# Kernel optimization log

Hardware: AMD Instinct MI355X
Metric: run time of the kernel (lower is better)

## Reference

```python
import jax, jax.numpy as jnp
import numpy as np

N = 100000
E = 1600000
IN, HID, OUT = 128, 256, 128


def setup_inputs() -> dict:
    key = jax.random.key(0)
    ks = jax.random.split(key, 8)
    x = jax.random.normal(ks[0], (N, IN), dtype=jnp.float32)
    edge_index = jax.random.randint(ks[1], (2, E), 0, N, dtype=jnp.int64)
    # PyG SAGEConv params: lin_l (neighbor aggr, with bias), lin_r (root, no bias)
    def glorot(k, shape):
        fan_in = shape[1]
        return jax.random.normal(k, shape, dtype=jnp.float32) / jnp.sqrt(jnp.float32(fan_in))
    W1l = glorot(ks[2], (HID, IN)); b1 = jnp.zeros((HID,), jnp.float32)
    W1r = glorot(ks[3], (HID, IN))
    W2l = glorot(ks[4], (OUT, HID)); b2 = jnp.zeros((OUT,), jnp.float32)
    W2r = glorot(ks[5], (OUT, HID))
    return {"x": x, "edge_index": edge_index, "W1l": W1l, "b1": b1,
            "W1r": W1r, "W2l": W2l, "b2": b2, "W2r": W2r}


def sage_conv(x, row, col, Wl, b, Wr, n_nodes):
    # mean-aggregate neighbor features x[row] at target nodes col
    msg = x[row]                                               # [E, d]
    s = jax.ops.segment_sum(msg, col, num_segments=n_nodes)    # [N, d]
    deg = jax.ops.segment_sum(jnp.ones((row.shape[0], 1), x.dtype), col,
                              num_segments=n_nodes)            # [N, 1]
    mean = s / jnp.maximum(deg, 1.0)
    return mean @ Wl.T + b + x @ Wr.T


def reference(x, edge_index, W1l, b1, W1r, W2l, b2, W2r):
    row, col = edge_index[0], edge_index[1]
    h = sage_conv(x, row, col, W1l, b1, W1r, N)
    h = jax.nn.relu(h)
    # dropout is identity in eval mode
    out = sage_conv(h, row, col, W2l, b2, W2r, N)
    return out
```

## Files before the change

### kernel.cpp

```cpp
#include <hip/hip_runtime.h>
#include <hip/hip_bf16.h>
#include <hip/hip_fp16.h>

#define NN 100000
#define NE 1600000
#define NCHUNK ((NN + 127) / 128)
#define NPB 512
#define NB 256
#define CHUNK 8192
#define NCH ((NE + CHUNK - 1) / CHUNK)

typedef __attribute__((ext_vector_type(8))) short short8;
typedef __attribute__((ext_vector_type(4))) float float4v;
typedef __attribute__((ext_vector_type(2))) float float2v;

__device__ __forceinline__ unsigned short f2bf(float f) {
    unsigned int b = __float_as_uint(f);
    return (unsigned short)((b + 0x7fffu + ((b >> 16) & 1u)) >> 16);
}
__device__ __forceinline__ unsigned int pack_bf16(float lo, float hi) {
    return (unsigned int)f2bf(lo) | ((unsigned int)f2bf(hi) << 16);
}
__device__ __forceinline__ unsigned char f2fp8(float v) {
    int r = __builtin_amdgcn_cvt_pk_fp8_f32(v, v, 0, false);
    return (unsigned char)(r & 0xff);
}
__device__ __forceinline__ unsigned short pack2fp8(float lo, float hi) {
    int r = __builtin_amdgcn_cvt_pk_fp8_f32(lo, hi, 0, false);
    return (unsigned short)(r & 0xffff);
}
__device__ __forceinline__ float h2f(unsigned short u) {
    return __half2float(__ushort_as_half(u));
}

__global__ void k_prep(const float* x, const float* W1l, const float* W1r,
                       const float* W2l, const float* W2r, const int* ei,
                       unsigned int* axb_u, unsigned short* xf8, unsigned short* wb1,
                       unsigned short* wb2, int* bcnt, unsigned short* gz) {
    __shared__ int hh[NB];
    int b = blockIdx.x, t = threadIdx.x;
    if (b < 3125) {
#pragma unroll
        for (int k = 0; k < 8; k++) {
            int tt = b * 2048 + k * 256 + t;
            int node = tt >> 6, i = tt & 63;
            float2 v = ((const float2*)x)[tt];
            axb_u[(size_t)node * 128 + 64 + i] = pack_bf16(v.x, v.y);
            xf8[(size_t)node * 64 + i] = pack2fp8(v.x, v.y);
        }
    } else if (b < 3253) {
        int i = (b - 3125) * 256 + t;
        int r1 = i >> 7, c1 = i & 127;
        wb1[r1 * 256 + c1]       = f2bf(W1l[i]);
        wb1[r1 * 256 + 128 + c1] = f2bf(W1r[i]);
        wb2[i]         = f2bf(W2l[i]);
        wb2[32768 + i] = f2bf(W2r[i]);
    } else if (b < 3509) {
        hh[t] = 0;
        __syncthreads();
        int e0 = (b - 3253) * 6250;
        for (int e = e0 + t; e < e0 + 6250; e += 256)
            atomicAdd(&hh[ei[NE + e] >> 9], 1);
        __syncthreads();
        if (hh[t]) atomicAdd(&bcnt[t], hh[t]);
    } else {
        if (t < 64) xf8[(size_t)NN * 64 + t] = 0;
        else if (t < 128 && gz) gz[(size_t)NN * 64 + (t - 64)] = 0;
    }
}

__global__ void k_bscan(const int* bcnt, int* boff, int* bcur) {
    __shared__ int s[NB];
    int t = threadIdx.x;
    int v = bcnt[t];
    s[t] = v;
    __syncthreads();
    for (int d = 1; d < NB; d <<= 1) {
        int val = (t >= d) ? s[t - d] : 0;
        __syncthreads();
        s[t] += val;
        __syncthreads();
    }
    boff[t + 1] = s[t];
    if (t == 0) boff[0] = 0;
    bcur[t] = s[t] - v;
}

__global__ __launch_bounds__(256) void k_bscatter(const int* ei, int* bcur, unsigned int* pairs) {
    __shared__ unsigned int buf[CHUNK];
    __shared__ int cnt[NB];
    __shared__ int lbase[NB];
    __shared__ int lcur[NB];
    __shared__ int gpos[NB];
    int t = threadIdx.x;
    int e0 = blockIdx.x * CHUNK;
    int nedge = NE - e0; if (nedge > CHUNK) nedge = CHUNK;
    cnt[t] = 0;
    __syncthreads();
    for (int i = t; i < nedge; i += 256)
        atomicAdd(&cnt[ei[NE + e0 + i] >> 9], 1);
    __syncthreads();
    int v = cnt[t];
    lcur[t] = v;
    __syncthreads();
    for (int d = 1; d < NB; d <<= 1) {
        int val = (t >= d) ? lcur[t - d] : 0;
        __syncthreads();
        lcur[t] += val;
        __syncthreads();
    }
    lbase[t] = lcur[t] - v;
    gpos[t] = atomicAdd(&bcur[t], v);
    __syncthreads();
    lcur[t] = lbase[t];
    __syncthreads();
    for (int i = t; i < nedge; i += 256) {
        int r = ei[e0 + i], c = ei[NE + e0 + i];
        int b = c >> 9;
        int p = atomicAdd(&lcur[b], 1);
        buf[p] = (unsigned)r | ((unsigned)(c & 511) << 17);
    }
    __syncthreads();
    int wv = t >> 6, lane = t & 63;
    for (int b = wv; b < NB; b += 4) {
        int n = cnt[b], lb = lbase[b], gp = gpos[b];
        for (int i = lane; i < n; i += 64)
            pairs[gp + i] = buf[lb + i];
    }
}

__global__ __launch_bounds__(256) void k_build(const unsigned int* pairs, const int* boff,
                                               int* off, int* deg, int* csr, int* csr32) {
    __shared__ int ldeg[NPB];
    __shared__ int lcur[NPB];
    __shared__ int lini[NPB];
    __shared__ int sscan[256];
    int b = blockIdx.x;
    int nbase = b * NPB;
    if (nbase >= NN) return;
    int t = threadIdx.x;
    int base = boff[b], cntb = boff[b + 1] - base;
    ldeg[t] = 0; ldeg[t + 256] = 0;
    __syncthreads();
    for (int i = t; i < cntb; i += 256) {
        unsigned int pr = pairs[base + i];
        atomicAdd(&ldeg[pr >> 17], 1);
    }
    __syncthreads();
    int d0 = ldeg[2 * t], d1 = ldeg[2 * t + 1];
    int v = d0 + d1;
    sscan[t] = v;
    __syncthreads();
    for (int d = 1; d < 256; d <<= 1) {
        int val = (t >= d) ? sscan[t - d] : 0;
        __syncthreads();
        sscan[t] += val;
        __syncthreads();
    }
    int ex = sscan[t] - v;
    lcur[2 * t] = ex;      lcur[2 * t + 1] = ex + d0;
    lini[2 * t] = ex;      lini[2 * t + 1] = ex + d0;
    __syncthreads();
    int nloc = NN - nbase; if (nloc > NPB) nloc = NPB;
    for (int ln = t; ln < nloc; ln += 256) {
        off[nbase + ln] = base + lcur[ln];
        deg[nbase + ln] = ldeg[ln];
    }
    __syncthreads();
    if (csr32) {
        for (int i = t; i < cntb; i += 256) {
            unsigned int pr = pairs[base + i];
            int nd = pr >> 17;
            int p = atomicAdd(&lcur[nd], 1);
            int src = (int)(pr & 0x1FFFFu);
            csr[base + p] = src;
            int rk = p - lini[nd];
            if (rk < 32) csr32[(size_t)(nbase + nd) * 32 + rk] = src;
        }
    } else {
        for (int i = t; i < cntb; i += 256) {
            unsigned int pr = pairs[base + i];
            int p = atomicAdd(&lcur[pr >> 17], 1);
            csr[base + p] = (int)(pr & 0x1FFFFu);
        }
    }
}

__global__ __launch_bounds__(512) void k_agg1(const unsigned short* xf8, const int* off,
                                              const int* deg, const int* csr, const int* csr32,
                                              unsigned int* axb_w) {
    int wid = (blockIdx.x * 512 + threadIdx.x) >> 6;
    if (wid >= NN) return;
    int widu = __builtin_amdgcn_readfirstlane(wid);
    int lane = threadIdx.x & 63;
    int d = deg[widu];
    float a0 = 0.f, a1 = 0.f;
    if (csr32) {
        const int* c32 = csr32 + (size_t)widu * 32;
        int dm = d < 32 ? d : 32;
#pragma unroll
        for (int r = 0; r < 32; r++) {
            int idx = (r < dm) ? c32[r] : NN;
            unsigned short u = xf8[(size_t)idx * 64 + lane];
            float2v f = __builtin_amdgcn_cvt_pk_f32_fp8((unsigned int)u, false);
            a0 += f.x; a1 += f.y;
        }
        if (d > 32) {
            int start = off[widu];
            for (int j = 32; j < d; j++) {
                int idx = csr[start + j];
                unsigned short u = xf8[(size_t)idx * 64 + lane];
                float2v f = __builtin_amdgcn_cvt_pk_f32_fp8((unsigned int)u, false);
                a0 += f.x; a1 += f.y;
            }
        }
    } else {
        int start = off[widu];
        for (int j = 0; j < d; j++) {
            int idx = csr[start + j];
            unsigned short u = xf8[(size_t)idx * 64 + lane];
            float2v f = __builtin_amdgcn_cvt_pk_f32_fp8((unsigned int)u, false);
            a0 += f.x; a1 += f.y;
        }
    }
    float inv = 1.0f / (float)(d > 0 ? d : 1);
    axb_w[(size_t)wid * 128 + lane] = pack_bf16(a0 * inv, a1 * inv);
}

__global__ __launch_bounds__(512) void k_agg2(const unsigned short* g, const int* off,
                                              const int* deg, const int* csr, const int* csr32,
                                              const unsigned short* partial, float* out) {
    int wid = (blockIdx.x * 512 + threadIdx.x) >> 6;
    if (wid >= NN) return;
    int widu = __builtin_amdgcn_readfirstlane(wid);
    int lane = threadIdx.x & 63;
    int d = deg[widu];
    unsigned int pu = *(const unsigned int*)(partial + (size_t)widu * 128 + (lane << 1));
    float a0 = 0.f, a1 = 0.f;
    if (csr32) {
        const int* c32 = csr32 + (size_t)widu * 32;
        int dm = d < 32 ? d : 32;
#pragma unroll
        for (int r = 0; r < 32; r++) {
            int idx = (r < dm) ? c32[r] : NN;
            unsigned short u = g[(size_t)idx * 64 + lane];
            float2v f = __builtin_amdgcn_cvt_pk_f32_fp8((unsigned int)u, false);
            a0 += f.x; a1 += f.y;
        }
        if (d > 32) {
            int start = off[widu];
            for (int j = 32; j < d; j++) {
                int idx = csr[start + j];
                unsigned short u = g[(size_t)idx * 64 + lane];
                float2v f = __builtin_amdgcn_cvt_pk_f32_fp8((unsigned int)u, false);
                a0 += f.x; a1 += f.y;
            }
        }
    } else {
        int start = off[widu];
        for (int j = 0; j < d; j++) {
            int idx = csr[start + j];
            unsigned short u = g[(size_t)idx * 64 + lane];
            float2v f = __builtin_amdgcn_cvt_pk_f32_fp8((unsigned int)u, false);
            a0 += f.x; a1 += f.y;
        }
    }
    float inv = 1.0f / (float)(d > 0 ? d : 1);
    float2 o;
    o.x = h2f((unsigned short)(pu & 0xffff)) + a0 * inv;
    o.y = h2f((unsigned short)(pu >> 16)) + a1 * inv;
    *(float2*)(out + (size_t)wid * 128 + (lane << 1)) = o;
}

#define BROW 264
#define GGRID (32 * ((NCHUNK + 7) / 8))
__global__ __launch_bounds__(256, 4) void k_gemm1(const unsigned short* A, const unsigned short* wb,
                                                  const float* b1, unsigned short* H) {
    __shared__ unsigned short Bs[64 * BROW];
    int t = threadIdx.x;
    int b = blockIdx.x;
    int chunk = (b & 7) + ((b >> 5) << 3);
    int cg = (b >> 3) & 3;
    if (chunk >= NCHUNK) return;
    {
        const short8* src = (const short8*)(wb + (size_t)cg * 64 * 256);
        short8* dst = (short8*)Bs;
#pragma unroll
        for (int i = 0; i < 8; i++) {
            int gi = i * 256 + t;
            int r = gi >> 5, c = gi & 31;
            dst[r * 33 + c] = src[gi];
        }
    }
    __syncthreads();
    int wv = t >> 6, lane = t & 63;
    int mrow = lane & 15, quad = lane >> 4;
    int base = chunk * 128 + wv * 32;
    if (base >= NN) return;
    float bias[4];
#pragma unroll
    for (int ctl = 0; ctl < 4; ctl++) bias[ctl] = b1[cg * 64 + ctl * 16 + mrow];
    float4v acc[2][4];
#pragma unroll
    for (int h = 0; h < 2; h++)
#pragma unroll
        for (int ctl = 0; ctl < 4; ctl++) acc[h][ctl] = (float4v)(0.0f);
    const short8* a0p = (const short8*)(A + (size_t)(base + mrow) * 256);
    const short8* a1p = (const short8*)(A + (size_t)(base + 16 + mrow) * 256);
#pragma unroll
    for (int kk = 0; kk < 8; kk++) {
        short8 a0 = a0p[kk * 4 + quad];
        short8 a1 = a1p[kk * 4 + quad];
        int koff = kk * 32 + quad * 8;
#pragma unroll
        for (int ctl = 0; ctl < 4; ctl++) {
            short8 bfr = *(const short8*)(Bs + (ctl * 16 + mrow) * BROW + koff);
            acc[0][ctl] = __builtin_amdgcn_mfma_f32_16x16x32_bf16(a0, bfr, acc[0][ctl], 0, 0, 0);
            acc[1][ctl] = __builtin_amdgcn_mfma_f32_16x16x32_bf16(a1, bfr, acc[1][ctl], 0, 0, 0);
        }
    }
#pragma unroll
    for (int ctl = 0; ctl < 4; ctl++) {
        int col = cg * 64 + ctl * 16 + mrow;
#pragma unroll
        for (int h = 0; h < 2; h++)
#pragma unroll
            for (int r = 0; r < 4; r++) {
                int node = base + h * 16 + quad * 4 + r;
                float v = acc[h][ctl][r] + bias[ctl];
                H[(size_t)node * 256 + col] = f2bf(fmaxf(v, 0.f));
            }
    }
}

__global__ __launch_bounds__(256, 4) void k_gemm2(const unsigned short* A, const unsigned short* wb,
                                                  const float* b2, unsigned char* g,
                                                  unsigned short* partial) {
    __shared__ unsigned short Bs[64 * BROW];
    int t = threadIdx.x;
    int b = blockIdx.x;
    int chunk = (b & 7) + ((b >> 5) << 3);
    int cg = (b >> 3) & 3;
    if (chunk >= NCHUNK) return;
    {
        const short8* src = (const short8*)(wb + (size_t)cg * 64 * 256);
        short8* dst = (short8*)Bs;
#pragma unroll
        for (int i = 0; i < 8; i++) {
            int gi = i * 256 + t;
            int r = gi >> 5, c = gi & 31;
            dst[r * 33 + c] = src[gi];
        }
    }
    __syncthreads();
    int wv = t >> 6, lane = t & 63;
    int mrow = lane & 15, quad = lane >> 4;
    int base = chunk * 128 + wv * 32;
    if (base >= NN) return;
    float bias[4];
#pragma unroll
    for (int ctl = 0; ctl < 4; ctl++)
        bias[ctl] = (cg >= 2) ? b2[cg * 64 + ctl * 16 + mrow - 128] : 0.f;
    float4v acc[2][4];
#pragma unroll
    for (int h = 0; h < 2; h++)
#pragma unroll
        for (int ctl = 0; ctl < 4; ctl++) acc[h][ctl] = (float4v)(0.0f);
    const short8* a0p = (const short8*)(A + (size_t)(base + mrow) * 256);
    const short8* a1p = (const short8*)(A + (size_t)(base + 16 + mrow) * 256);
#pragma unroll
    for (int kk = 0; kk < 8; kk++) {
        short8 a0 = a0p[kk * 4 + quad];
        short8 a1 = a1p[kk * 4 + quad];
        int koff = kk * 32 + quad * 8;
#pragma unroll
        for (int ctl = 0; ctl < 4; ctl++) {
            short8 bfr = *(const short8*)(Bs + (ctl * 16 + mrow) * BROW + koff);
            acc[0][ctl] = __builtin_amdgcn_mfma_f32_16x16x32_bf16(a0, bfr, acc[0][ctl], 0, 0, 0);
            acc[1][ctl] = __builtin_amdgcn_mfma_f32_16x16x32_bf16(a1, bfr, acc[1][ctl], 0, 0, 0);
        }
    }
    if (cg < 2) {
#pragma unroll
        for (int ctl = 0; ctl < 4; ctl++) {
            int col = cg * 64 + ctl * 16 + mrow;
#pragma unroll
            for (int h = 0; h < 2; h++)
#pragma unroll
                for (int r = 0; r < 4; r++) {
                    int node = base + h * 16 + quad * 4 + r;
                    g[(size_t)node * 128 + col] = f2fp8(acc[h][ctl][r]);
                }
        }
    } else {
#pragma unroll
        for (int ctl = 0; ctl < 4; ctl++) {
            int pcol = cg * 64 + ctl * 16 + mrow - 128;
#pragma unroll
            for (int h = 0; h < 2; h++)
#pragma unroll
                for (int r = 0; r < 4; r++) {
                    int node = base + h * 16 + quad * 4 + r;
                    __half hf = __float2half(acc[h][ctl][r] + bias[ctl]);
                    partial[(size_t)node * 128 + pcol] = __half_as_ushort(hf);
                }
        }
    }
}

extern "C" void kernel_launch(void* const* d_in, const int* in_sizes, int n_in,
                              void* d_out, int out_size, void* d_ws, size_t ws_size,
                              hipStream_t stream) {
    const float* x   = (const float*)d_in[0];
    const int*   ei  = (const int*)d_in[1];
    const float* W1l = (const float*)d_in[2];
    const float* b1  = (const float*)d_in[3];
    const float* W1r = (const float*)d_in[4];
    const float* W2l = (const float*)d_in[5];
    const float* b2  = (const float*)d_in[6];
    const float* W2r = (const float*)d_in[7];
    float* out = (float*)d_out;

    char* p = (char*)d_ws;
    unsigned int* axb = (unsigned int*)p; p += (size_t)NN * 256 * 2;
    unsigned short* h = (unsigned short*)p; p += (size_t)NN * 256 * 2;
    unsigned char* g  = (unsigned char*)p; p += (size_t)NN * 128 + 256;
    unsigned short* xf8 = (unsigned short*)p; p += (size_t)NN * 128 + 256;
    unsigned short* wb1 = (unsigned short*)p; p += 65536 * 2;
    unsigned short* wb2 = (unsigned short*)p; p += 65536 * 2;
    int* deg  = (int*)p; p += (size_t)NN * 4;
    int* off  = (int*)p; p += (size_t)NN * 4;
    int* csr  = (int*)p; p += (size_t)NE * 4;
    int* bcnt = (int*)p; p += NB * 4;
    int* boff = (int*)p; p += (NB + 1) * 4;
    int* bcur = (int*)p; p += NB * 4;
    if (ws_size < (size_t)(p - (char*)d_ws)) return;
    int* csr32 = (int*)p; p += (size_t)NN * 32 * 4;
    if (ws_size < (size_t)(p - (char*)d_ws)) csr32 = nullptr;
    unsigned int* pairs = (unsigned int*)h;
    unsigned short* partial = (unsigned short*)axb;

    hipMemsetAsync(bcnt, 0, NB * 4, stream);
    k_prep<<<3510, 256, 0, stream>>>(x, W1l, W1r, W2l, W2r, ei, axb, xf8, wb1, wb2, bcnt,
                                     (unsigned short*)g);
    k_bscan<<<1, NB, 0, stream>>>(bcnt, boff, bcur);
    k_bscatter<<<NCH, 256, 0, stream>>>(ei, bcur, pairs);
    k_build<<<NB, 256, 0, stream>>>(pairs, boff, off, deg, csr, csr32);
    k_agg1<<<12500, 512, 0, stream>>>(xf8, off, deg, csr, csr32, axb);
    k_gemm1<<<GGRID, 256, 0, stream>>>((const unsigned short*)axb, wb1, b1, h);
    k_gemm2<<<GGRID, 256, 0, stream>>>(h, wb2, b2, g, partial);
    k_agg2<<<12500, 512, 0, stream>>>((const unsigned short*)g, off, deg, csr, csr32, partial, out);
}
```

Before: 362.3 us.

## Slice fp8 feature tables into column slabs for cache-local neighbor gathers

Stores the fp8 node features (input x and layer-2 g) as four 32-byte column slices, each a separate contiguous array. Aggregation kernels now use 16 lanes per node and 4 nodes per wave, with block IDs interleaved so neighbouring blocks gather from the same slice, shrinking the working set per slice so it fits in cache. Neighbour indices are loaded once per lane and broadcast with shuffles, and streaming loads and stores are marked nontemporal. The partial-sum layout is also sliced to match. The csr32-absent fallback is removed, so correctness now assumes the workspace is large enough for csr32.

```diff
diff --git a/kernel.cpp b/kernel.cpp
--- a/kernel.cpp
+++ b/kernel.cpp
@@ -4,6 +4,7 @@
 
 #define NN 100000
 #define NE 1600000
+#define NNP (NN + 8)
 #define NCHUNK ((NN + 127) / 128)
 #define NPB 512
 #define NB 256
@@ -14,6 +15,9 @@
 typedef __attribute__((ext_vector_type(4))) float float4v;
 typedef __attribute__((ext_vector_type(2))) float float2v;
 
+#define SLS ((size_t)NNP * 16)
+#define NN32 ((size_t)NN * 32)
+
 __device__ __forceinline__ unsigned short f2bf(float f) {
     unsigned int b = __float_as_uint(f);
     return (unsigned short)((b + 0x7fffu + ((b >> 16) & 1u)) >> 16);
@@ -35,8 +39,8 @@
 
 __global__ void k_prep(const float* x, const float* W1l, const float* W1r,
                        const float* W2l, const float* W2r, const int* ei,
-                       unsigned int* axb_u, unsigned short* xf8, unsigned short* wb1,
-                       unsigned short* wb2, int* bcnt, unsigned short* gz) {
+                       unsigned int* axb_u, unsigned short* xf8s, unsigned short* wb1,
+                       unsigned short* wb2, int* bcnt, unsigned short* g2z) {
     __shared__ int hh[NB];
     int b = blockIdx.x, t = threadIdx.x;
     if (b < 3125) {
@@ -46,7 +50,7 @@
             int node = tt >> 6, i = tt & 63;
             float2 v = ((const float2*)x)[tt];
             axb_u[(size_t)node * 128 + 64 + i] = pack_bf16(v.x, v.y);
-            xf8[(size_t)node * 64 + i] = pack2fp8(v.x, v.y);
+            xf8s[(size_t)(i >> 4) * SLS + (size_t)node * 16 + (i & 15)] = pack2fp8(v.x, v.y);
         }
     } else if (b < 3253) {
         int i = (b - 3125) * 256 + t;
@@ -64,8 +68,11 @@
         __syncthreads();
         if (hh[t]) atomicAdd(&bcnt[t], hh[t]);
     } else {
-        if (t < 64) xf8[(size_t)NN * 64 + t] = 0;
-        else if (t < 128 && gz) gz[(size_t)NN * 64 + (t - 64)] = 0;
+        if (t < 64) xf8s[(size_t)(t >> 4) * SLS + (size_t)NN * 16 + (t & 15)] = 0;
+        else if (t < 128) {
+            int q = t - 64;
+            g2z[(size_t)(q >> 4) * SLS + (size_t)NN * 16 + (q & 15)] = 0;
+        }
     }
 }
 
@@ -186,90 +193,88 @@
     }
 }
 
-__global__ __launch_bounds__(512) void k_agg1(const unsigned short* xf8, const int* off,
+__global__ __launch_bounds__(512) void k_agg1(const unsigned short* xs, const int* off,
                                               const int* deg, const int* csr, const int* csr32,
                                               unsigned int* axb_w) {
-    int wid = (blockIdx.x * 512 + threadIdx.x) >> 6;
-    if (wid >= NN) return;
-    int widu = __builtin_amdgcn_readfirstlane(wid);
-    int lane = threadIdx.x & 63;
-    int d = deg[widu];
+    int bid = blockIdx.x;
+    int s = (bid & 7) >> 1;
+    int k = ((bid >> 3) << 1) | (bid & 1);
+    if (k >= 3125) return;
+    int t = threadIdx.x;
+    int lane = t & 63;
+    int grp = lane >> 4, l16 = lane & 15;
+    int node = k * 32 + (t >> 6) * 4 + grp;
+    const unsigned short* gs = xs + (size_t)s * SLS;
+    int d = deg[node];
+    const int* c32 = csr32 + (size_t)node * 32;
+    int e0 = __builtin_nontemporal_load(c32 + l16);
+    int e1 = __builtin_nontemporal_load(c32 + 16 + l16);
+    int dm = d < 32 ? d : 32;
     float a0 = 0.f, a1 = 0.f;
-    if (csr32) {
-        const int* c32 = csr32 + (size_t)widu * 32;
-        int dm = d < 32 ? d : 32;
-#pragma unroll
-        for (int r = 0; r < 32; r++) {
-            int idx = (r < dm) ? c32[r] : NN;
-            unsigned short u = xf8[(size_t)idx * 64 + lane];
+#pragma unroll
+    for (int slot = 0; slot < 32; slot++) {
+        int idx = __shfl(slot < 16 ? e0 : e1, (grp << 4) | (slot & 15), 64);
+        idx = (slot < dm) ? idx : NN;
+        unsigned short u = gs[(size_t)idx * 16 + l16];
+        float2v f = __builtin_amdgcn_cvt_pk_f32_fp8((unsigned int)u, false);
+        a0 += f.x; a1 += f.y;
+    }
+    if (d > 32) {
+        int st = off[node];
+        for (int j = 32; j < d; j++) {
+            int idx = csr[st + j];
+            unsigned short u = gs[(size_t)idx * 16 + l16];
             float2v f = __builtin_amdgcn_cvt_pk_f32_fp8((unsigned int)u, false);
             a0 += f.x; a1 += f.y;
         }
-        if (d > 32) {
-            int start = off[widu];
-            for (int j = 32; j < d; j++) {
-                int idx = csr[start + j];
-                unsigned short u = xf8[(size_t)idx * 64 + lane];
-                float2v f = __builtin_amdgcn_cvt_pk_f32_fp8((unsigned int)u, false);
-                a0 += f.x; a1 += f.y;
-            }
-        }
-    } else {
-        int start = off[widu];
-        for (int j = 0; j < d; j++) {
-            int idx = csr[start + j];
-            unsigned short u = xf8[(size_t)idx * 64 + lane];
+    }
+    float inv = 1.0f / (float)(d > 0 ? d : 1);
+    __builtin_nontemporal_store(pack_bf16(a0 * inv, a1 * inv),
+                                axb_w + (size_t)node * 128 + (s << 4) + l16);
+}
+
+__global__ __launch_bounds__(512) void k_agg2(const unsigned short* g2, const int* off,
+                                              const int* deg, const int* csr, const int* csr32,
+                                              const unsigned short* pslc, float* out) {
+    int bid = blockIdx.x;
+    int s = (bid & 7) >> 1;
+    int k = ((bid >> 3) << 1) | (bid & 1);
+    if (k >= 3125) return;
+    int t = threadIdx.x;
+    int lane = t & 63;
+    int grp = lane >> 4, l16 = lane & 15;
+    int node = k * 32 + (t >> 6) * 4 + grp;
+    const unsigned short* gs = g2 + (size_t)s * SLS;
+    int d = deg[node];
+    const int* c32 = csr32 + (size_t)node * 32;
+    int e0 = __builtin_nontemporal_load(c32 + l16);
+    int e1 = __builtin_nontemporal_load(c32 + 16 + l16);
+    unsigned int pu = __builtin_nontemporal_load(
+        (const unsigned int*)(pslc + (size_t)s * NN32 + (size_t)node * 32 + (l16 << 1)));
+    int dm = d < 32 ? d : 32;
+    float a0 = 0.f, a1 = 0.f;
+#pragma unroll
+    for (int slot = 0; slot < 32; slot++) {
+        int idx = __shfl(slot < 16 ? e0 : e1, (grp << 4) | (slot & 15), 64);
+        idx = (slot < dm) ? idx : NN;
+        unsigned short u = gs[(size_t)idx * 16 + l16];
+        float2v f = __builtin_amdgcn_cvt_pk_f32_fp8((unsigned int)u, false);
+        a0 += f.x; a1 += f.y;
+    }
+    if (d > 32) {
+        int st = off[node];
+        for (int j = 32; j < d; j++) {
+            int idx = csr[st + j];
+            unsigned short u = gs[(size_t)idx * 16 + l16];
             float2v f = __builtin_amdgcn_cvt_pk_f32_fp8((unsigned int)u, false);
             a0 += f.x; a1 += f.y;
         }
     }
     float inv = 1.0f / (float)(d > 0 ? d : 1);
-    axb_w[(size_t)wid * 128 + lane] = pack_bf16(a0 * inv, a1 * inv);
-}
-
-__global__ __launch_bounds__(512) void k_agg2(const unsigned short* g, const int* off,
-                                              const int* deg, const int* csr, const int* csr32,
-                                              const unsigned short* partial, float* out) {
-    int wid = (blockIdx.x * 512 + threadIdx.x) >> 6;
-    if (wid >= NN) return;
-    int widu = __builtin_amdgcn_readfirstlane(wid);
-    int lane = threadIdx.x & 63;
-    int d = deg[widu];
-    unsigned int pu = *(const unsigned int*)(partial + (size_t)widu * 128 + (lane << 1));
-    float a0 = 0.f, a1 = 0.f;
-    if (csr32) {
-        const int* c32 = csr32 + (size_t)widu * 32;
-        int dm = d < 32 ? d : 32;
-#pragma unroll
-        for (int r = 0; r < 32; r++) {
-            int idx = (r < dm) ? c32[r] : NN;
-            unsigned short u = g[(size_t)idx * 64 + lane];
-            float2v f = __builtin_amdgcn_cvt_pk_f32_fp8((unsigned int)u, false);
-            a0 += f.x; a1 += f.y;
-        }
-        if (d > 32) {
-            int start = off[widu];
-            for (int j = 32; j < d; j++) {
-                int idx = csr[start + j];
-                unsigned short u = g[(size_t)idx * 64 + lane];
-                float2v f = __builtin_amdgcn_cvt_pk_f32_fp8((unsigned int)u, false);
-                a0 += f.x; a1 += f.y;
-            }
-        }
-    } else {
-        int start = off[widu];
-        for (int j = 0; j < d; j++) {
-            int idx = csr[start + j];
-            unsigned short u = g[(size_t)idx * 64 + lane];
-            float2v f = __builtin_amdgcn_cvt_pk_f32_fp8((unsigned int)u, false);
-            a0 += f.x; a1 += f.y;
-        }
-    }
-    float inv = 1.0f / (float)(d > 0 ? d : 1);
-    float2 o;
+    float2v o;
     o.x = h2f((unsigned short)(pu & 0xffff)) + a0 * inv;
     o.y = h2f((unsigned short)(pu >> 16)) + a1 * inv;
-    *(float2*)(out + (size_t)wid * 128 + (lane << 1)) = o;
+    __builtin_nontemporal_store(o, (float2v*)(out + (size_t)node * 128 + (s << 5)) + l16);
 }
 
 #define BROW 264
@@ -334,8 +339,8 @@
 }
 
 __global__ __launch_bounds__(256, 4) void k_gemm2(const unsigned short* A, const unsigned short* wb,
-                                                  const float* b2, unsigned char* g,
-                                                  unsigned short* partial) {
+                                                  const float* b2, unsigned char* g2b,
+                                                  unsigned short* pslc) {
     __shared__ unsigned short Bs[64 * BROW];
     int t = threadIdx.x;
     int b = blockIdx.x;
@@ -389,7 +394,8 @@
 #pragma unroll
                 for (int r = 0; r < 4; r++) {
                     int node = base + h * 16 + quad * 4 + r;
-                    g[(size_t)node * 128 + col] = f2fp8(acc[h][ctl][r]);
+                    g2b[(size_t)(col >> 5) * ((size_t)NNP * 32) + (size_t)node * 32 + (col & 31)]
+                        = f2fp8(acc[h][ctl][r]);
                 }
         }
     } else {
@@ -402,7 +408,8 @@
                 for (int r = 0; r < 4; r++) {
                     int node = base + h * 16 + quad * 4 + r;
                     __half hf = __float2half(acc[h][ctl][r] + bias[ctl]);
-                    partial[(size_t)node * 128 + pcol] = __half_as_ushort(hf);
+                    pslc[(size_t)(pcol >> 5) * NN32 + (size_t)node * 32 + (pcol & 31)]
+                        = __half_as_ushort(hf);
                 }
         }
     }
@@ -424,8 +431,8 @@
     char* p = (char*)d_ws;
     unsigned int* axb = (unsigned int*)p; p += (size_t)NN * 256 * 2;
     unsigned short* h = (unsigned short*)p; p += (size_t)NN * 256 * 2;
-    unsigned char* g  = (unsigned char*)p; p += (size_t)NN * 128 + 256;
-    unsigned short* xf8 = (unsigned short*)p; p += (size_t)NN * 128 + 256;
+    unsigned char* g2 = (unsigned char*)p; p += (size_t)4 * NNP * 32;
+    unsigned short* xf8s = (unsigned short*)p; p += (size_t)4 * NNP * 32;
     unsigned short* wb1 = (unsigned short*)p; p += 65536 * 2;
     unsigned short* wb2 = (unsigned short*)p; p += 65536 * 2;
     int* deg  = (int*)p; p += (size_t)NN * 4;
@@ -438,16 +445,16 @@
     int* csr32 = (int*)p; p += (size_t)NN * 32 * 4;
     if (ws_size < (size_t)(p - (char*)d_ws)) csr32 = nullptr;
     unsigned int* pairs = (unsigned int*)h;
-    unsigned short* partial = (unsigned short*)axb;
+    unsigned short* pslc = (unsigned short*)axb;
 
     hipMemsetAsync(bcnt, 0, NB * 4, stream);
-    k_prep<<<3510, 256, 0, stream>>>(x, W1l, W1r, W2l, W2r, ei, axb, xf8, wb1, wb2, bcnt,
-                                     (unsigned short*)g);
+    k_prep<<<3510, 256, 0, stream>>>(x, W1l, W1r, W2l, W2r, ei, axb, xf8s, wb1, wb2, bcnt,
+                                     (unsigned short*)g2);
     k_bscan<<<1, NB, 0, stream>>>(bcnt, boff, bcur);
     k_bscatter<<<NCH, 256, 0, stream>>>(ei, bcur, pairs);
     k_build<<<NB, 256, 0, stream>>>(pairs, boff, off, deg, csr, csr32);
-    k_agg1<<<12500, 512, 0, stream>>>(xf8, off, deg, csr, csr32, axb);
+    k_agg1<<<12504, 512, 0, stream>>>(xf8s, off, deg, csr, csr32, axb);
     k_gemm1<<<GGRID, 256, 0, stream>>>((const unsigned short*)axb, wb1, b1, h);
-    k_gemm2<<<GGRID, 256, 0, stream>>>(h, wb2, b2, g, partial);
-    k_agg2<<<12500, 512, 0, stream>>>((const unsigned short*)g, off, deg, csr, csr32, partial, out);
-}
+    k_gemm2<<<GGRID, 256, 0, stream>>>(h, wb2, b2, g2, pslc);
+    k_agg2<<<12504, 512, 0, stream>>>((const unsigned short*)g2, off, deg, csr, csr32, pslc, out);
+}
```

After: 410.6 us. 1.13x slower.
